# Kernel optimization log

Hardware: AMD Instinct MI355X
Metric: run time of the kernel (lower is better)

## Reference

```python
import jax, jax.numpy as jnp
import numpy as np

NH = 16          # num_attention_heads
NOPE = 128       # qk_nope_head_dim
ROPE = 64        # qk_rope_head_dim
QHD = NOPE + ROPE  # q_head_dim = 192
VD = 128         # v_head_dim
QLR = 1536       # q_lora_rank
KVLR = 512       # kv_lora_rank
HID = 2048
B, S = 1, 2048
THETA = 10000.0
EPS = 1e-6


def rms_norm(x, w, eps=EPS):
    xf = x.astype(jnp.float32)
    var = jnp.mean(xf * xf, axis=-1, keepdims=True)
    return (w * (xf * jax.lax.rsqrt(var + eps)).astype(x.dtype))


def _deinterleave(x):
    # view(..., d//2, 2).transpose(-1, -2).reshape(..., d): evens then odds
    return jnp.concatenate([x[..., 0::2], x[..., 1::2]], axis=-1)


def _rotate_half(x):
    h = x.shape[-1] // 2
    return jnp.concatenate([-x[..., h:], x[..., :h]], axis=-1)


def setup_inputs() -> dict:
    key = jax.random.key(0)
    ks = jax.random.split(key, 6)
    s = 0.02
    return {
        'hidden_states': jax.random.normal(ks[0], (B, S, HID), jnp.float32),
        'position_ids': jnp.arange(S, dtype=jnp.int32)[None, :],
        'Wqa': jax.random.normal(ks[1], (HID, QLR), jnp.float32) * s,
        'qa_ln_w': jnp.ones((QLR,), jnp.float32),
        'Wqb': jax.random.normal(ks[2], (QLR, NH * QHD), jnp.float32) * s,
        'Wkva': jax.random.normal(ks[3], (HID, KVLR + ROPE), jnp.float32) * s,
        'kv_ln_w': jnp.ones((KVLR,), jnp.float32),
        'Wkvb': jax.random.normal(ks[4], (KVLR, NH * (NOPE + VD)), jnp.float32) * s,
        'Wo': jax.random.normal(ks[5], (NH * VD, HID), jnp.float32) * s,
    }


def reference(hidden_states, position_ids, Wqa, qa_ln_w, Wqb, Wkva, kv_ln_w, Wkvb, Wo):
    b, s, _ = hidden_states.shape
    # Q path: low-rank down -> RMSNorm -> up
    q = rms_norm(hidden_states @ Wqa, qa_ln_w) @ Wqb
    q = q.reshape(b, s, NH, QHD).transpose(0, 2, 1, 3)          # (b,h,s,192)
    q_nope, q_pe = q[..., :NOPE], q[..., NOPE:]
    # KV path: compressed kv + shared rope key
    ckv = hidden_states @ Wkva                                   # (b,s,576)
    c_kv, k_pe = ckv[..., :KVLR], ckv[..., KVLR:]
    k_pe = k_pe.reshape(b, s, 1, ROPE).transpose(0, 2, 1, 3)     # (b,1,s,64)
    kv = rms_norm(c_kv, kv_ln_w) @ Wkvb
    kv = kv.reshape(b, s, NH, NOPE + VD).transpose(0, 2, 1, 3)   # (b,h,s,256)
    k_nope, v = kv[..., :NOPE], kv[..., NOPE:]
    # partial RoPE on the 64-dim rope slices
    inv_freq = 1.0 / (THETA ** (jnp.arange(0, ROPE, 2, dtype=jnp.float32) / ROPE))
    t = jnp.arange(s, dtype=jnp.float32)
    emb = jnp.concatenate([jnp.outer(t, inv_freq)] * 2, axis=-1)  # (s,64)
    cos = jnp.cos(emb)[position_ids][:, None]                     # (b,1,s,64)
    sin = jnp.sin(emb)[position_ids][:, None]
    q_pe = _deinterleave(q_pe)
    k_pe = _deinterleave(k_pe)
    q_pe = q_pe * cos + _rotate_half(q_pe) * sin
    k_pe = k_pe * cos + _rotate_half(k_pe) * sin
    query = jnp.concatenate([q_nope, q_pe], axis=-1)                       # (b,h,s,192)
    key = jnp.concatenate([k_nope, jnp.broadcast_to(k_pe, (b, NH, s, ROPE))], axis=-1)
    # causal attention, softmax_scale = q_head_dim**-0.5
    scale = QHD ** (-0.5)
    scores = jnp.einsum('bhqd,bhkd->bhqk', query, key) * scale
    mask = jnp.tril(jnp.ones((s, s), dtype=bool))
    scores = jnp.where(mask, scores, jnp.finfo(scores.dtype).min)
    probs = jax.nn.softmax(scores, axis=-1)
    attn = jnp.einsum('bhqk,bhkd->bhqd', probs, v)               # (b,h,s,128)
    out = attn.transpose(0, 2, 1, 3).reshape(b, s, NH * VD) @ Wo  # (b,s,hid)
    return out
```

## Files before the change

### kernel.cpp

```cpp
#include <hip/hip_runtime.h>
#include <hip/hip_bf16.h>

typedef unsigned short u16;
typedef _Float16 h16;
typedef h16 h16x8 __attribute__((ext_vector_type(8)));
typedef h16 h16x4 __attribute__((ext_vector_type(4)));
typedef float f32x4 __attribute__((ext_vector_type(4)));

#define S_LEN 2048
#define QLR   1536
#define KVLR  512
#define NHEAD 16
#define QHD   192
#define QHS   200
#define NOPE  128
#define VDIM  128
#define SCALE 0.07216878364870322f
#define FREQC (-0.4152410118609203f)

__device__ __forceinline__ void gld16(const h16* g, h16* l){
  __builtin_amdgcn_global_load_lds((__attribute__((address_space(1))) const void*)g,
                                   (__attribute__((address_space(3))) void*)l, 16, 0, 0);
}

__global__ __launch_bounds__(256) void k_cvt(const float* __restrict__ in, h16* __restrict__ out, int n4){
  int i = blockIdx.x * 256 + threadIdx.x;
  if (i < n4){
    float4 v = ((const float4*)in)[i];
    h16x4 o = { (h16)v.x, (h16)v.y, (h16)v.z, (h16)v.w };
    ((h16x4*)out)[i] = o;
  }
}

__global__ __launch_bounds__(256) void k_tc(const float* __restrict__ W, h16* __restrict__ WT, int K, int N){
  __shared__ float t[32][33];
  int k0 = blockIdx.y * 32, n0 = blockIdx.x * 32;
  int tid = threadIdx.x;
  int r  = tid >> 3, c4 = (tid & 7) * 4;
  float4 v = *(const float4*)(W + (size_t)(k0 + r) * N + n0 + c4);
  t[r][c4] = v.x; t[r][c4+1] = v.y; t[r][c4+2] = v.z; t[r][c4+3] = v.w;
  __syncthreads();
  h16x4 o = { (h16)t[c4][r], (h16)t[c4+1][r], (h16)t[c4+2][r], (h16)t[c4+3][r] };
  *(h16x4*)(WT + (size_t)(n0 + r) * K + k0 + c4) = o;
}

__device__ __forceinline__ void gemm_core(const h16* __restrict__ A, const h16* __restrict__ B,
    int K, int m0, int n0, h16* As, h16* Bs, f32x4 (&acc)[4][4]){
  const int tid = threadIdx.x;
  const int lane = tid & 63, quad = lane >> 4, lr = lane & 15;
  const int wid = tid >> 6;
  const int wr = (wid >> 1) * 64, wc = (wid & 1) * 64;
  const int sr = tid >> 2, scc = (tid & 3) * 8;
  const h16* Ag = A + (size_t)(m0 + sr) * K + scc;
  const h16* Bg = B + (size_t)(n0 + sr) * K + scc;
  for (int kt = 0; kt < K; kt += 32){
    gld16(Ag + kt,                 &As[tid * 8]);
    gld16(Ag + (size_t)64*K + kt,  &As[2048 + tid * 8]);
    gld16(Bg + kt,                 &Bs[tid * 8]);
    gld16(Bg + (size_t)64*K + kt,  &Bs[2048 + tid * 8]);
    __syncthreads();
    h16x8 af[4], bfr[4];
#pragma unroll
    for (int r = 0; r < 4; r++) af[r]  = *(const h16x8*)&As[(wr + r*16 + lr) * 32 + quad * 8];
#pragma unroll
    for (int c = 0; c < 4; c++) bfr[c] = *(const h16x8*)&Bs[(wc + c*16 + lr) * 32 + quad * 8];
#pragma unroll
    for (int r = 0; r < 4; r++)
#pragma unroll
      for (int c = 0; c < 4; c++)
        acc[r][c] = __builtin_amdgcn_mfma_f32_16x16x32_f16(af[r], bfr[c], acc[r][c], 0, 0, 0);
    __syncthreads();
  }
}

template<bool OF32>
__global__ __launch_bounds__(256) void k_gemm(const h16* __restrict__ A, const h16* __restrict__ B,
                                              void* __restrict__ Cv, int N, int K){
  __shared__ __attribute__((aligned(16))) h16 As[128*32];
  __shared__ __attribute__((aligned(16))) h16 Bs[128*32];
  const int m0 = blockIdx.y * 128, n0 = blockIdx.x * 128;
  f32x4 acc[4][4] = {};
  gemm_core(A, B, K, m0, n0, As, Bs, acc);
  const int lane = threadIdx.x & 63, quad = lane >> 4, lr = lane & 15;
  const int wid = threadIdx.x >> 6;
  const int wr = (wid >> 1) * 64, wc = (wid & 1) * 64;
#pragma unroll
  for (int r = 0; r < 4; r++)
#pragma unroll
    for (int c = 0; c < 4; c++){
      int row = m0 + wr + r*16 + quad*4;
      int col = n0 + wc + c*16 + lr;
#pragma unroll
      for (int i = 0; i < 4; i++){
        float val = acc[r][c][i];
        if (OF32) ((float*)Cv)[(size_t)(row + i) * N + col] = val;
        else      ((h16*)Cv)[(size_t)(row + i) * N + col] = (h16)val;
      }
    }
}

__global__ __launch_bounds__(256) void k_norm(const h16* __restrict__ Cc,
      const float* __restrict__ qw, const float* __restrict__ kw, const int* __restrict__ pos_ids,
      h16* __restrict__ qln, h16* __restrict__ kvln, h16* __restrict__ kpe,
      float* __restrict__ cst, float* __restrict__ snt){
  const int s = blockIdx.x, tid = threadIdx.x;
  __shared__ float red[8];
  const h16* c1 = Cc + (size_t)s * 2176;
  float v[6]; float ss = 0.f;
#pragma unroll
  for (int i = 0; i < 6; i++){ v[i] = (float)c1[tid + i*256]; ss += v[i]*v[i]; }
  for (int off = 32; off > 0; off >>= 1) ss += __shfl_down(ss, off);
  if ((tid & 63) == 0) red[tid >> 6] = ss;
  __syncthreads();
  float rq = rsqrtf((red[0]+red[1]+red[2]+red[3]) / (float)QLR + 1e-6f);
#pragma unroll
  for (int i = 0; i < 6; i++)
    qln[(size_t)s * QLR + tid + i*256] = (h16)(qw[tid + i*256] * v[i] * rq);

  const h16* ck = c1 + QLR;
  float w0 = (float)ck[tid], w1 = (float)ck[tid + 256];
  float ss2 = w0*w0 + w1*w1;
  for (int off = 32; off > 0; off >>= 1) ss2 += __shfl_down(ss2, off);
  if ((tid & 63) == 0) red[4 + (tid >> 6)] = ss2;
  __syncthreads();
  float rk = rsqrtf((red[4]+red[5]+red[6]+red[7]) / (float)KVLR + 1e-6f);
  kvln[(size_t)s * KVLR + tid]       = (h16)(kw[tid] * w0 * rk);
  kvln[(size_t)s * KVLR + tid + 256] = (h16)(kw[tid + 256] * w1 * rk);

  if (tid < 32){
    int d = tid;
    float x = (float)ck[KVLR + 2*d];
    float y = (float)ck[KVLR + 2*d + 1];
    float a = (float)pos_ids[s] * exp2f(FREQC * (float)d);
    float cs = cosf(a), sn = sinf(a);
    cst[s*32 + d] = cs; snt[s*32 + d] = sn;
    kpe[(size_t)s*64 + d]      = (h16)(x*cs - y*sn);
    kpe[(size_t)s*64 + 32 + d] = (h16)(y*cs + x*sn);
  }
}

__global__ __launch_bounds__(256) void k_asm(const h16* __restrict__ Qm, const h16* __restrict__ KVm,
      const h16* __restrict__ kpe, const float* __restrict__ cst, const float* __restrict__ snt,
      h16* __restrict__ Qh, h16* __restrict__ Kh, h16* __restrict__ VT){
  const int t = blockIdx.x, h = blockIdx.y, tid = threadIdx.x;
  const int s0 = t * 64;
#pragma unroll
  for (int it = 0; it < 6; it++){
    int cid = it*256 + tid;
    int r = cid / 24, c8 = (cid - r*24) * 8;
    int rr = s0 + r;
    const h16* in = Qm + (size_t)rr*3072 + h*192;
    h16* outr = Qh + ((size_t)h*S_LEN + rr)*QHS;
    h16x8 v = *(const h16x8*)(in + c8);
    if (c8 < 128){
      h16x8 o;
#pragma unroll
      for (int e = 0; e < 8; e++) o[e] = (h16)((float)v[e] * SCALE);
      *(h16x8*)(outr + c8) = o;
    } else {
      int k4 = (c8 - 128) >> 1;
      h16x4 xo, yo;
#pragma unroll
      for (int m2 = 0; m2 < 4; m2++){
        float x = (float)v[2*m2], y = (float)v[2*m2+1];
        float cs = cst[rr*32 + k4 + m2], sn = snt[rr*32 + k4 + m2];
        xo[m2] = (h16)((x*cs - y*sn) * SCALE);
        yo[m2] = (h16)((y*cs + x*sn) * SCALE);
      }
      *(h16x4*)(outr + 128 + k4) = xo;
      *(h16x4*)(outr + 160 + k4) = yo;
    }
  }
#pragma unroll
  for (int it = 0; it < 6; it++){
    int cid = it*256 + tid;
    int r = cid / 24, c8 = (cid - r*24) * 8;
    int rr = s0 + r;
    h16* outr = Kh + ((size_t)h*S_LEN + rr)*QHS;
    if (c8 < 128){
      h16x8 v = *(const h16x8*)(KVm + (size_t)rr*4096 + h*256 + c8);
      *(h16x8*)(outr + c8) = v;
    } else {
      h16x8 v = *(const h16x8*)(kpe + (size_t)rr*64 + (c8 - 128));
      *(h16x8*)(outr + c8) = v;
    }
  }
  {
    int dv = tid >> 1, half = tid & 1;
    const h16* vin = KVm + h*256 + 128 + dv;
    h16* vout = VT + ((size_t)(h*VDIM + dv))*S_LEN + s0;
#pragma unroll
    for (int k = 0; k < 4; k++){
      h16x8 o;
#pragma unroll
      for (int e = 0; e < 8; e++)
        o[e] = vin[(size_t)(s0 + half*32 + k*8 + e) * 4096];
      *(h16x8*)(vout + ((half*32 + k*8 + 8*(dv & 7)) & 63)) = o;
    }
  }
}

__global__ __launch_bounds__(256) void k_flash(const h16* __restrict__ Qh, const h16* __restrict__ Kh,
      const h16* __restrict__ VT, h16* __restrict__ O){
  const int tile = 31 - blockIdx.x;
  const int h = blockIdx.y;
  const int m0 = tile * 64;
  __shared__ __attribute__((aligned(16))) h16 Ksm[64*QHS];
  __shared__ __attribute__((aligned(16))) h16 Vsm[144*64];
  __shared__ __attribute__((aligned(16))) h16 Psm[64*72];
  const int tid = threadIdx.x, wid = tid >> 6, lane = tid & 63, quad = lane >> 4, lr = lane & 15;

  {
    h16x4 one4 = { (h16)1.f, (h16)1.f, (h16)1.f, (h16)1.f };
    *(h16x4*)&Vsm[128*64 + tid*4] = one4;
  }

  const h16* Qg = Qh + ((size_t)h*S_LEN + m0)*QHS;
#pragma unroll
  for (int i = 0; i < 6; i++) gld16(Qg + i*2048 + tid*8, &Ksm[i*2048 + tid*8]);
  if (wid == 0) gld16(Qg + 12288 + lane*8, &Ksm[12288 + lane*8]);
  __syncthreads();
  h16x8 qf[6];
#pragma unroll
  for (int ks = 0; ks < 6; ks++)
    qf[ks] = *(const h16x8*)&Ksm[(wid*16 + lr)*QHS + ks*32 + quad*8];
  __syncthreads();

  float mst[4];
  f32x4 oacc[9] = {};
#pragma unroll
  for (int i = 0; i < 4; i++) mst[i] = -1e30f;

  for (int j = 0; j <= tile; ++j){
    const h16* Kg = Kh + ((size_t)h*S_LEN + j*64)*QHS;
#pragma unroll
    for (int i = 0; i < 6; i++) gld16(Kg + i*2048 + tid*8, &Ksm[i*2048 + tid*8]);
    if (wid == 0) gld16(Kg + 12288 + lane*8, &Ksm[12288 + lane*8]);
    const h16* Vg = VT + (size_t)h * VDIM * S_LEN + (size_t)j * 64;
#pragma unroll
    for (int i = 0; i < 4; i++)
      gld16(Vg + (size_t)(i*32 + (tid >> 3)) * S_LEN + (tid & 7)*8, &Vsm[i*2048 + tid*8]);
    __syncthreads();

    f32x4 sc[4] = {};
#pragma unroll
    for (int ks = 0; ks < 6; ks++)
#pragma unroll
      for (int ct = 0; ct < 4; ct++){
        h16x8 kf = *(const h16x8*)&Ksm[(ct*16 + lr)*QHS + ks*32 + quad*8];
        sc[ct] = __builtin_amdgcn_mfma_f32_16x16x32_f16(qf[ks], kf, sc[ct], 0,0,0);
      }

    if (j == tile){
#pragma unroll
      for (int ct = 0; ct < 4; ct++)
#pragma unroll
        for (int i = 0; i < 4; i++)
          if (ct*16 + lr > wid*16 + quad*4 + i) sc[ct][i] = -1e30f;
    }

    float al[4];
#pragma unroll
    for (int i = 0; i < 4; i++){
      float m = fmaxf(fmaxf(sc[0][i], sc[1][i]), fmaxf(sc[2][i], sc[3][i]));
#pragma unroll
      for (int off = 1; off < 16; off <<= 1) m = fmaxf(m, __shfl_xor(m, off));
      float mn = fmaxf(mst[i], m);
      al[i] = __expf(mst[i] - mn);
      mst[i] = mn;
    }
#pragma unroll
    for (int ct = 0; ct < 4; ct++)
#pragma unroll
      for (int i = 0; i < 4; i++)
        Psm[(wid*16 + quad*4 + i)*72 + ct*16 + lr] = (h16)__expf(sc[ct][i] - mst[i]);
#pragma unroll
    for (int oc = 0; oc < 9; oc++)
#pragma unroll
      for (int i = 0; i < 4; i++) oacc[oc][i] *= al[i];

#pragma unroll
    for (int ks2 = 0; ks2 < 2; ks2++){
      h16x8 pf = *(const h16x8*)&Psm[(wid*16 + lr)*72 + ks2*32 + quad*8];
#pragma unroll
      for (int oc = 0; oc < 9; oc++){
        int cv = (ks2*32 + quad*8 + 8*(lr & 7)) & 63;
        h16x8 vf = *(const h16x8*)&Vsm[(oc*16 + lr)*64 + cv];
        oacc[oc] = __builtin_amdgcn_mfma_f32_16x16x32_f16(pf, vf, oacc[oc], 0,0,0);
      }
    }
    __syncthreads();
  }

  float inv[4];
#pragma unroll
  for (int i = 0; i < 4; i++) inv[i] = 1.f / oacc[8][i];
#pragma unroll
  for (int oc = 0; oc < 8; oc++){
    int col = h*VDIM + oc*16 + lr;
#pragma unroll
    for (int i = 0; i < 4; i++){
      int row = m0 + wid*16 + quad*4 + i;
      O[(size_t)row * (NHEAD*VDIM) + col] = (h16)(oacc[oc][i] * inv[i]);
    }
  }
}

extern "C" void kernel_launch(void* const* d_in, const int* in_sizes, int n_in,
                              void* d_out, int out_size, void* d_ws, size_t ws_size,
                              hipStream_t stream){
  const float* hidden = (const float*)d_in[0];
  const int*   pos    = (const int*)  d_in[1];
  const float* Wqa    = (const float*)d_in[2];
  const float* qaw    = (const float*)d_in[3];
  const float* Wqb    = (const float*)d_in[4];
  const float* Wkva   = (const float*)d_in[5];
  const float* kvw    = (const float*)d_in[6];
  const float* Wkvb   = (const float*)d_in[7];
  const float* Wo     = (const float*)d_in[8];

  h16* ws = (h16*)d_ws;
  size_t off = 0;
  auto take = [&](size_t n){ h16* p = ws + off; off += n; return p; };
  h16* hb    = take(2048ull * 2048);
  h16* Wc    = take(2176ull * 2048);
  h16* WqbT  = take(3072ull * 1536);
  h16* WkvbT = take(4096ull * 512);
  h16* WoT   = take(2048ull * 2048);
  h16* Ccomb = take(2048ull * 2176);
  h16* qln   = take(2048ull * 1536);
  h16* kvln  = take(2048ull * 512);
  h16* kpe   = take(2048ull * 64);
  float* cst = (float*)take(2048ull * 64);
  float* snt = (float*)take(2048ull * 64);
  h16* Qm    = take(2048ull * 3072);
  h16* KVm   = take(2048ull * 4096);
  h16* Qh    = take(16ull * 2048 * QHS);
  h16* Kh    = take(16ull * 2048 * QHS);
  h16* VT    = take(16ull * 128 * 2048);
  h16* Ob    = hb;

  k_cvt<<<4096, 256, 0, stream>>>(hidden, hb, 1048576);
  k_tc<<<dim3(48, 64), 256, 0, stream>>>(Wqa,  Wc,                 2048, 1536);
  k_tc<<<dim3(18, 64), 256, 0, stream>>>(Wkva, Wc + 1536ull*2048,  2048, 576);
  k_tc<<<dim3(96, 48), 256, 0, stream>>>(Wqb,  WqbT,  1536, 3072);
  k_tc<<<dim3(128,16), 256, 0, stream>>>(Wkvb, WkvbT, 512,  4096);
  k_tc<<<dim3(64, 64), 256, 0, stream>>>(Wo,   WoT,   2048, 2048);

  k_gemm<false><<<dim3(17, 16), 256, 0, stream>>>(hb, Wc, Ccomb, 2176, 2048);
  k_norm<<<2048, 256, 0, stream>>>(Ccomb, qaw, kvw, pos, qln, kvln, kpe, cst, snt);
  k_gemm<false><<<dim3(24, 16), 256, 0, stream>>>(qln,  WqbT,  Qm,  3072, 1536);
  k_gemm<false><<<dim3(32, 16), 256, 0, stream>>>(kvln, WkvbT, KVm, 4096, 512);
  k_asm<<<dim3(32, 16), 256, 0, stream>>>(Qm, KVm, kpe, cst, snt, Qh, Kh, VT);
  k_flash<<<dim3(32, 16), 256, 0, stream>>>(Qh, Kh, VT, Ob);
  k_gemm<true><<<dim3(16, 16), 256, 0, stream>>>(Ob, WoT, d_out, 2048, 2048);
}
```

Measured before the change: 395.7 us.

## Split flash attention over KV chunks with a combine kernel; widen transpose tiles

The flash kernel now splits each query tile's causal KV range into up to four chunks of eight key blocks, launched along a third grid dimension. Partial unnormalized outputs and per-row max and sum values go to reused workspace buffers, and a new combine kernel merges them with log-sum-exp weights. This is meant to even out the triangular causal workload and raise the number of active blocks (512 before). In exchange it adds extra global traffic, rounds partial outputs to fp16, and adds a kernel launch. The weight transpose kernel also moves to 64x64 tiles with 16-byte stores.

After: 398.6 us. No clear change (+0.7%).

```diff
diff --git a/kernel.cpp b/kernel.cpp
--- a/kernel.cpp
+++ b/kernel.cpp
@@ -33,15 +33,23 @@
 }
 
 __global__ __launch_bounds__(256) void k_tc(const float* __restrict__ W, h16* __restrict__ WT, int K, int N){
-  __shared__ float t[32][33];
-  int k0 = blockIdx.y * 32, n0 = blockIdx.x * 32;
+  __shared__ float t[64][65];
+  int k0 = blockIdx.y * 64, n0 = blockIdx.x * 64;
   int tid = threadIdx.x;
-  int r  = tid >> 3, c4 = (tid & 7) * 4;
-  float4 v = *(const float4*)(W + (size_t)(k0 + r) * N + n0 + c4);
-  t[r][c4] = v.x; t[r][c4+1] = v.y; t[r][c4+2] = v.z; t[r][c4+3] = v.w;
+  int r = tid >> 4, c4 = (tid & 15) * 4;
+#pragma unroll
+  for (int it = 0; it < 4; it++){
+    float4 v = *(const float4*)(W + (size_t)(k0 + it*16 + r) * N + n0 + c4);
+    t[it*16+r][c4] = v.x; t[it*16+r][c4+1] = v.y; t[it*16+r][c4+2] = v.z; t[it*16+r][c4+3] = v.w;
+  }
   __syncthreads();
-  h16x4 o = { (h16)t[c4][r], (h16)t[c4+1][r], (h16)t[c4+2][r], (h16)t[c4+3][r] };
-  *(h16x4*)(WT + (size_t)(n0 + r) * K + k0 + c4) = o;
+  int n = tid >> 2, k16 = (tid & 3) * 16;
+  h16x8 o0, o1;
+#pragma unroll
+  for (int e = 0; e < 8; e++){ o0[e] = (h16)t[k16 + e][n]; o1[e] = (h16)t[k16 + 8 + e][n]; }
+  h16* dst = WT + (size_t)(n0 + n) * K + k0 + k16;
+  *(h16x8*)dst = o0;
+  *(h16x8*)(dst + 8) = o1;
 }
 
 __device__ __forceinline__ void gemm_core(const h16* __restrict__ A, const h16* __restrict__ B,
@@ -201,9 +209,13 @@
 }
 
 __global__ __launch_bounds__(256) void k_flash(const h16* __restrict__ Qh, const h16* __restrict__ Kh,
-      const h16* __restrict__ VT, h16* __restrict__ O){
+      const h16* __restrict__ VT, h16* __restrict__ Opart, float* __restrict__ ml){
   const int tile = 31 - blockIdx.x;
   const int h = blockIdx.y;
+  const int p = blockIdx.z;
+  const int jlo = p * 8;
+  if (jlo > tile) return;
+  const int jhi = min(jlo + 8, tile + 1);
   const int m0 = tile * 64;
   __shared__ __attribute__((aligned(16))) h16 Ksm[64*QHS];
   __shared__ __attribute__((aligned(16))) h16 Vsm[144*64];
@@ -231,7 +243,7 @@
 #pragma unroll
   for (int i = 0; i < 4; i++) mst[i] = -1e30f;
 
-  for (int j = 0; j <= tile; ++j){
+  for (int j = jlo; j < jhi; ++j){
     const h16* Kg = Kh + ((size_t)h*S_LEN + j*64)*QHS;
 #pragma unroll
     for (int i = 0; i < 6; i++) gld16(Kg + i*2048 + tid*8, &Ksm[i*2048 + tid*8]);
@@ -292,17 +304,48 @@
     __syncthreads();
   }
 
-  float inv[4];
-#pragma unroll
-  for (int i = 0; i < 4; i++) inv[i] = 1.f / oacc[8][i];
-#pragma unroll
-  for (int oc = 0; oc < 8; oc++){
-    int col = h*VDIM + oc*16 + lr;
+  const int part = (tile*NHEAD + h)*4 + p;
+  h16* Op = Opart + (size_t)part * 8192;
+#pragma unroll
+  for (int oc = 0; oc < 8; oc++)
+#pragma unroll
+    for (int i = 0; i < 4; i++)
+      Op[(wid*16 + quad*4 + i)*128 + oc*16 + lr] = (h16)oacc[oc][i];
+  if (lr == 0){
 #pragma unroll
     for (int i = 0; i < 4; i++){
-      int row = m0 + wid*16 + quad*4 + i;
-      O[(size_t)row * (NHEAD*VDIM) + col] = (h16)(oacc[oc][i] * inv[i]);
-    }
+      int r = wid*16 + quad*4 + i;
+      ml[(size_t)part*128 + r*2]     = mst[i];
+      ml[(size_t)part*128 + r*2 + 1] = oacc[8][i];
+    }
+  }
+}
+
+__global__ __launch_bounds__(256) void k_comb(const h16* __restrict__ Opart, const float* __restrict__ ml,
+                                              h16* __restrict__ Ob){
+  const int t = blockIdx.x, h = blockIdx.y, tid = threadIdx.x;
+  const int P = t/8 + 1;
+  const int r = tid >> 2, c0 = (tid & 3) * 32;
+  const int base = (t*NHEAD + h)*4;
+  float w[4]; float M = -1e30f, denom = 0.f;
+  for (int p = 0; p < P; p++) M = fmaxf(M, ml[(size_t)(base+p)*128 + r*2]);
+  for (int p = 0; p < P; p++){
+    w[p] = __expf(ml[(size_t)(base+p)*128 + r*2] - M);
+    denom += w[p] * ml[(size_t)(base+p)*128 + r*2 + 1];
+  }
+  float inv = 1.f / denom;
+#pragma unroll
+  for (int ch = 0; ch < 4; ch++){
+    float a[8] = {};
+    for (int p = 0; p < P; p++){
+      h16x8 v = *(const h16x8*)&Opart[(size_t)(base+p)*8192 + r*128 + c0 + ch*8];
+#pragma unroll
+      for (int e = 0; e < 8; e++) a[e] += w[p] * (float)v[e];
+    }
+    h16x8 o;
+#pragma unroll
+    for (int e = 0; e < 8; e++) o[e] = (h16)(a[e] * inv);
+    *(h16x8*)&Ob[((size_t)(t*64 + r))*(NHEAD*VDIM) + h*VDIM + c0 + ch*8] = o;
   }
 }
 
@@ -339,19 +382,22 @@
   h16* Kh    = take(16ull * 2048 * QHS);
   h16* VT    = take(16ull * 128 * 2048);
   h16* Ob    = hb;
+  h16*   Opart = qln;
+  float* mlbuf = (float*)Wc;
 
   k_cvt<<<4096, 256, 0, stream>>>(hidden, hb, 1048576);
-  k_tc<<<dim3(48, 64), 256, 0, stream>>>(Wqa,  Wc,                 2048, 1536);
-  k_tc<<<dim3(18, 64), 256, 0, stream>>>(Wkva, Wc + 1536ull*2048,  2048, 576);
-  k_tc<<<dim3(96, 48), 256, 0, stream>>>(Wqb,  WqbT,  1536, 3072);
-  k_tc<<<dim3(128,16), 256, 0, stream>>>(Wkvb, WkvbT, 512,  4096);
-  k_tc<<<dim3(64, 64), 256, 0, stream>>>(Wo,   WoT,   2048, 2048);
+  k_tc<<<dim3(24, 32), 256, 0, stream>>>(Wqa,  Wc,                 2048, 1536);
+  k_tc<<<dim3( 9, 32), 256, 0, stream>>>(Wkva, Wc + 1536ull*2048,  2048, 576);
+  k_tc<<<dim3(48, 24), 256, 0, stream>>>(Wqb,  WqbT,  1536, 3072);
+  k_tc<<<dim3(64,  8), 256, 0, stream>>>(Wkvb, WkvbT, 512,  4096);
+  k_tc<<<dim3(32, 32), 256, 0, stream>>>(Wo,   WoT,   2048, 2048);
 
   k_gemm<false><<<dim3(17, 16), 256, 0, stream>>>(hb, Wc, Ccomb, 2176, 2048);
   k_norm<<<2048, 256, 0, stream>>>(Ccomb, qaw, kvw, pos, qln, kvln, kpe, cst, snt);
   k_gemm<false><<<dim3(24, 16), 256, 0, stream>>>(qln,  WqbT,  Qm,  3072, 1536);
   k_gemm<false><<<dim3(32, 16), 256, 0, stream>>>(kvln, WkvbT, KVm, 4096, 512);
   k_asm<<<dim3(32, 16), 256, 0, stream>>>(Qm, KVm, kpe, cst, snt, Qh, Kh, VT);
-  k_flash<<<dim3(32, 16), 256, 0, stream>>>(Qh, Kh, VT, Ob);
+  k_flash<<<dim3(32, 16, 4), 256, 0, stream>>>(Qh, Kh, VT, Opart, mlbuf);
+  k_comb<<<dim3(32, 16), 256, 0, stream>>>(Opart, mlbuf, Ob);
   k_gemm<true><<<dim3(16, 16), 256, 0, stream>>>(Ob, WoT, d_out, 2048, 2048);
 }
```
